# Optimization experiments

Measured on AMD Instinct MI355X. Metric: run time of the kernel, lower is better.

The kernel has to match this reference:

```python
import jax, jax.numpy as jnp
import numpy as np

N_NODES = 50000
N_EDGES = 1500000
D = 512
LN_EPS = 1e-5


def setup_inputs() -> dict:
    key = jax.random.key(0)
    ks = jax.random.split(key, 8)
    scale = 1.0 / np.sqrt(D)
    return {
        "node_feature": jax.random.normal(ks[0], (N_NODES, D), dtype=jnp.float32),
        "edge_index": jax.random.randint(ks[1], (2, N_EDGES), 0, N_NODES, dtype=jnp.int32),
        "W_l": jax.random.uniform(ks[2], (D, D), jnp.float32, -scale, scale),  # neighbor lin
        "b_l": jnp.zeros((D,), jnp.float32),
        "W_r": jax.random.uniform(ks[3], (D, D), jnp.float32, -scale, scale),  # root lin (no bias)
        "gamma": jnp.ones((D,), jnp.float32),
        "beta": jnp.zeros((D,), jnp.float32),
    }


def _layer_norm(x, gamma, beta):
    mu = jnp.mean(x, axis=-1, keepdims=True)
    var = jnp.mean(jnp.square(x - mu), axis=-1, keepdims=True)
    return (x - mu) * jax.lax.rsqrt(var + LN_EPS) * gamma + beta


def reference(node_feature, edge_index, W_l, b_l, W_r, gamma, beta):
    n = node_feature.shape[0]
    residual = node_feature
    h = _layer_norm(node_feature, gamma, beta)
    src, dst = edge_index[0], edge_index[1]
    # mean-aggregate source features at destinations (gather + segment scatter)
    summed = jax.ops.segment_sum(h[src], dst, num_segments=n)  # [N, D]
    cnt = jax.ops.segment_sum(jnp.ones((src.shape[0],), h.dtype), dst, num_segments=n)
    mean = summed / jnp.maximum(cnt, 1.0)[:, None]
    # SAGEConv: lin_l(aggregated) + lin_r(root); bias on lin_l
    out = mean @ W_l.T + b_l + h @ W_r.T
    out = jax.nn.relu(out)
    return out + residual
```

## Files before the change

### kernel.cpp

```cpp
#include <hip/hip_runtime.h>


#define D_DIM 512

typedef __bf16 bf16x8 __attribute__((ext_vector_type(8)));
typedef float f32x4 __attribute__((ext_vector_type(4)));

__device__ __forceinline__ unsigned short f2bf(float f) {
  unsigned u = __float_as_uint(f);
  u += 0x7fffu + ((u >> 16) & 1u);
  return (unsigned short)(u >> 16);
}
__device__ __forceinline__ float bflo(unsigned u) { return __uint_as_float(u << 16); }
__device__ __forceinline__ float bfhi(unsigned u) { return __uint_as_float(u & 0xffff0000u); }
__device__ __forceinline__ unsigned packbf2(float lo, float hi) {
  return (unsigned)f2bf(lo) | ((unsigned)f2bf(hi) << 16);
}

__global__ void ln_kernel(const float* __restrict__ x, const float* __restrict__ gamma,
                          const float* __restrict__ beta, unsigned short* __restrict__ Acat,
                          int n) {
  int lane = threadIdx.x & 63;
  int row = blockIdx.x * 4 + (threadIdx.x >> 6);
  if (row >= n) return;
  const float* xr = x + (size_t)row * D_DIM + lane * 8;
  float4 a = *(const float4*)xr;
  float4 b = *(const float4*)(xr + 4);
  float sum = a.x + a.y + a.z + a.w + b.x + b.y + b.z + b.w;
  float sq = a.x * a.x + a.y * a.y + a.z * a.z + a.w * a.w +
             b.x * b.x + b.y * b.y + b.z * b.z + b.w * b.w;
#pragma unroll
  for (int m = 1; m < 64; m <<= 1) {
    sum += __shfl_xor(sum, m, 64);
    sq  += __shfl_xor(sq, m, 64);
  }
  float mu = sum * (1.0f / D_DIM);
  float var = sq * (1.0f / D_DIM) - mu * mu;
  float rs = rsqrtf(var + 1e-5f);
  const float* gp = gamma + lane * 8;
  const float* bp = beta + lane * 8;
  float4 g0 = *(const float4*)gp, g1 = *(const float4*)(gp + 4);
  float4 e0 = *(const float4*)bp, e1 = *(const float4*)(bp + 4);
  float h0 = (a.x - mu) * rs * g0.x + e0.x;
  float h1 = (a.y - mu) * rs * g0.y + e0.y;
  float h2 = (a.z - mu) * rs * g0.z + e0.z;
  float h3 = (a.w - mu) * rs * g0.w + e0.w;
  float h4 = (b.x - mu) * rs * g1.x + e1.x;
  float h5 = (b.y - mu) * rs * g1.y + e1.y;
  float h6 = (b.z - mu) * rs * g1.z + e1.z;
  float h7 = (b.w - mu) * rs * g1.w + e1.w;
  uint4 st = { packbf2(h0, h1), packbf2(h2, h3), packbf2(h4, h5), packbf2(h6, h7) };
  *(uint4*)(Acat + (size_t)row * 1024 + 512 + lane * 8) = st;
}

__global__ void wconv_kernel(const float* __restrict__ Wl, const float* __restrict__ Wr,
                             unsigned short* __restrict__ Wcat) {
  int id = blockIdx.x * 256 + threadIdx.x;
  int j = id >> 9, k = id & 511;
  Wcat[(size_t)j * 1024 + k] = f2bf(Wl[id]);
  Wcat[(size_t)j * 1024 + 512 + k] = f2bf(Wr[id]);
}

__global__ void zero_kernel(int* __restrict__ p, int n) {
  int i = blockIdx.x * 256 + threadIdx.x;
  if (i < n) p[i] = 0;
}

__global__ void hist_kernel(const int* __restrict__ dst, int nE, int* __restrict__ cnt) {
  int e = blockIdx.x * 256 + threadIdx.x;
  if (e < nE) atomicAdd(&cnt[dst[e]], 1);
}

__global__ void scan1_kernel(const int* __restrict__ cnt, int n,
                             int* __restrict__ excl, int* __restrict__ bsums) {
  __shared__ int wsum[16];
  int gid = blockIdx.x * 1024 + threadIdx.x;
  int lane = threadIdx.x & 63, wave = threadIdx.x >> 6;
  int v = (gid < n) ? cnt[gid] : 0;
  int s = v;
#pragma unroll
  for (int d = 1; d < 64; d <<= 1) {
    int t = __shfl_up(s, d, 64);
    if (lane >= d) s += t;
  }
  if (lane == 63) wsum[wave] = s;
  __syncthreads();
  if (wave == 0) {
    int ws = (lane < 16) ? wsum[lane] : 0;
#pragma unroll
    for (int d = 1; d < 16; d <<= 1) {
      int t = __shfl_up(ws, d, 64);
      if (lane >= d) ws += t;
    }
    if (lane < 16) wsum[lane] = ws;
  }
  __syncthreads();
  int incl = s + ((wave > 0) ? wsum[wave - 1] : 0);
  if (gid < n) excl[gid] = incl - v;
  if (threadIdx.x == 1023) bsums[blockIdx.x] = incl;
}

__global__ void scan2_kernel(int* __restrict__ bsums, int nb) {
  int lane = threadIdx.x;
  int v = (lane < nb) ? bsums[lane] : 0;
  int s = v;
#pragma unroll
  for (int d = 1; d < 64; d <<= 1) {
    int t = __shfl_up(s, d, 64);
    if (lane >= d) s += t;
  }
  if (lane < nb) bsums[lane] = s - v;
}

__global__ void scan3_kernel(int* __restrict__ rowst, int* __restrict__ cur,
                             const int* __restrict__ bsums, int n, int nE) {
  int gid = blockIdx.x * 1024 + threadIdx.x;
  if (gid < n) {
    int r = rowst[gid] + bsums[blockIdx.x];
    rowst[gid] = r;
    cur[gid] = r;
  }
  if (gid == 0) rowst[n] = nE;
}

__global__ void scatter_kernel(const int* __restrict__ src, const int* __restrict__ dst,
                               int nE, int* __restrict__ cur, int* __restrict__ sorted_src) {
  int e = blockIdx.x * 256 + threadIdx.x;
  if (e < nE) {
    int p = atomicAdd(&cur[dst[e]], 1);
    sorted_src[p] = src[e];
  }
}

__device__ __forceinline__ void acc_row(float* acc, uint4 r) {
  acc[0] += bflo(r.x); acc[1] += bfhi(r.x);
  acc[2] += bflo(r.y); acc[3] += bfhi(r.y);
  acc[4] += bflo(r.z); acc[5] += bfhi(r.z);
  acc[6] += bflo(r.w); acc[7] += bfhi(r.w);
}

__global__ void agg_kernel(unsigned short* __restrict__ Acat,
                           const int* __restrict__ rowst,
                           const int* __restrict__ sorted_src, int n) {
  int lane = threadIdx.x & 63;
  int node = blockIdx.x * 4 + (threadIdx.x >> 6);
  if (node >= n) return;
  int s0 = rowst[node], s1 = rowst[node + 1];
  float acc[8] = {0.f, 0.f, 0.f, 0.f, 0.f, 0.f, 0.f, 0.f};
  const unsigned short* hbase = Acat + 512 + lane * 8;
  int e = s0;
  for (; e + 3 < s1; e += 4) {
    int i0 = sorted_src[e], i1 = sorted_src[e + 1];
    int i2 = sorted_src[e + 2], i3 = sorted_src[e + 3];
    uint4 r0 = *(const uint4*)(hbase + (size_t)i0 * 1024);
    uint4 r1 = *(const uint4*)(hbase + (size_t)i1 * 1024);
    uint4 r2 = *(const uint4*)(hbase + (size_t)i2 * 1024);
    uint4 r3 = *(const uint4*)(hbase + (size_t)i3 * 1024);
    acc_row(acc, r0); acc_row(acc, r1); acc_row(acc, r2); acc_row(acc, r3);
  }
  for (; e < s1; ++e) {
    int i0 = sorted_src[e];
    uint4 r0 = *(const uint4*)(hbase + (size_t)i0 * 1024);
    acc_row(acc, r0);
  }
  int deg = s1 - s0;
  float sc = (deg > 0) ? (1.0f / (float)deg) : 0.0f;
  uint4 st = { packbf2(acc[0] * sc, acc[1] * sc), packbf2(acc[2] * sc, acc[3] * sc),
               packbf2(acc[4] * sc, acc[5] * sc), packbf2(acc[6] * sc, acc[7] * sc) };
  *(uint4*)(Acat + (size_t)node * 1024 + lane * 8) = st;
}

__device__ __forceinline__ void async16(const unsigned short* g, char* lds) {
  __builtin_amdgcn_global_load_lds((const __attribute__((address_space(1))) void*)g,
                                   (__attribute__((address_space(3))) void*)lds, 16, 0, 0);
}

__global__ __launch_bounds__(256) void gemm_kernel(
    const unsigned short* __restrict__ A,
    const unsigned short* __restrict__ B,
    const float* __restrict__ bias,
    const float* __restrict__ residual,
    float* __restrict__ out, int M) {
  __shared__ unsigned short sA[128 * 32];
  __shared__ unsigned short sB[128 * 32];
  const int K = 1024;
  int t = threadIdx.x;
  int lane = t & 63, wave = t >> 6;
  int quad = lane >> 4, l16 = lane & 15;
  int mb = blockIdx.x >> 2, nb = blockIdx.x & 3;
  int mBase = mb * 128, nBase = nb * 128;
  int wm = (wave & 1) * 64, wn = (wave >> 1) * 64;

  const unsigned short* gA = A + (size_t)(mBase + (t >> 2)) * K + (t & 3) * 8;
  const unsigned short* gB = B + (size_t)(nBase + (t >> 2)) * K + (t & 3) * 8;
  char* lA0 = (char*)sA + wave * 1024;
  char* lA1 = (char*)sA + 4096 + wave * 1024;
  char* lB0 = (char*)sB + wave * 1024;
  char* lB1 = (char*)sB + 4096 + wave * 1024;

  f32x4 acc[4][4] = {};

  for (int ks = 0; ks < K; ks += 32) {
    __syncthreads();
    async16(gA + ks, lA0);
    async16(gA + (size_t)64 * K + ks, lA1);
    async16(gB + ks, lB0);
    async16(gB + (size_t)64 * K + ks, lB1);
    __syncthreads();
    bf16x8 af[4], bf[4];
#pragma unroll
    for (int i = 0; i < 4; ++i)
      af[i] = *(const bf16x8*)(sA + (wm + i * 16 + l16) * 32 + quad * 8);
#pragma unroll
    for (int j = 0; j < 4; ++j)
      bf[j] = *(const bf16x8*)(sB + (wn + j * 16 + l16) * 32 + quad * 8);
#pragma unroll
    for (int i = 0; i < 4; ++i)
#pragma unroll
      for (int j = 0; j < 4; ++j)
        acc[i][j] = __builtin_amdgcn_mfma_f32_16x16x32_bf16(af[i], bf[j], acc[i][j], 0, 0, 0);
  }

  float biasv[4];
#pragma unroll
  for (int j = 0; j < 4; ++j) biasv[j] = bias[nBase + wn + j * 16 + l16];
#pragma unroll
  for (int i = 0; i < 4; ++i) {
    int gr0 = mBase + wm + i * 16 + quad * 4;
#pragma unroll
    for (int j = 0; j < 4; ++j) {
      int col = nBase + wn + j * 16 + l16;
#pragma unroll
      for (int r = 0; r < 4; ++r) {
        int gr = gr0 + r;
        if (gr < M) {
          size_t idx = (size_t)gr * D_DIM + col;
          float v = acc[i][j][r] + biasv[j];
          out[idx] = fmaxf(v, 0.0f) + residual[idx];
        }
      }
    }
  }
}

extern "C" void kernel_launch(void* const* d_in, const int* in_sizes, int n_in,
                              void* d_out, int out_size, void* d_ws, size_t ws_size,
                              hipStream_t stream) {
  const float* x = (const float*)d_in[0];
  const int* ei = (const int*)d_in[1];
  const float* Wl = (const float*)d_in[2];
  const float* bl = (const float*)d_in[3];
  const float* Wr = (const float*)d_in[4];
  const float* gamma = (const float*)d_in[5];
  const float* beta = (const float*)d_in[6];
  float* out = (float*)d_out;

  int n = in_sizes[0] / D_DIM;
  int nE = in_sizes[1] / 2;
  const int* src = ei;
  const int* dstv = ei + nE;
  int Mpad = (n + 127) & ~127;

  char* w = (char*)d_ws;
  size_t off = 0;
  auto carve = [&](size_t bytes) {
    char* p = w + off;
    off += (bytes + 255) & ~(size_t)255;
    return p;
  };
  unsigned short* Acat = (unsigned short*)carve((size_t)Mpad * 1024 * 2);
  unsigned short* Wcat = (unsigned short*)carve((size_t)512 * 1024 * 2);
  int* sorted = (int*)carve((size_t)nE * 4);
  int* cnt = (int*)carve((size_t)n * 4);
  int* rowst = (int*)carve((size_t)(n + 1) * 4);
  int* cur = (int*)carve((size_t)n * 4);
  int* bsums = (int*)carve(1024);
  if (off > ws_size) return;

  int nbScan = (n + 1023) / 1024;

  ln_kernel<<<(n + 3) / 4, 256, 0, stream>>>(x, gamma, beta, Acat, n);
  wconv_kernel<<<(512 * 512) / 256, 256, 0, stream>>>(Wl, Wr, Wcat);
  zero_kernel<<<(n + 255) / 256, 256, 0, stream>>>(cnt, n);
  hist_kernel<<<(nE + 255) / 256, 256, 0, stream>>>(dstv, nE, cnt);
  scan1_kernel<<<nbScan, 1024, 0, stream>>>(cnt, n, rowst, bsums);
  scan2_kernel<<<1, 64, 0, stream>>>(bsums, nbScan);
  scan3_kernel<<<nbScan, 1024, 0, stream>>>(rowst, cur, bsums, n, nE);
  scatter_kernel<<<(nE + 255) / 256, 256, 0, stream>>>(src, dstv, nE, cur, sorted);
  agg_kernel<<<(n + 3) / 4, 256, 0, stream>>>(Acat, rowst, sorted, n);
  gemm_kernel<<<(Mpad / 128) * 4, 256, 0, stream>>>(Acat, Wcat, bl, x, out, n);
}
```

Measured before the change: 736.4 us.

## Gather neighbor features from an FP8 copy of normalized features during aggregation

```diff
diff --git a/kernel.cpp b/kernel.cpp
--- a/kernel.cpp
+++ b/kernel.cpp
@@ -5,6 +5,7 @@
 
 typedef __bf16 bf16x8 __attribute__((ext_vector_type(8)));
 typedef float f32x4 __attribute__((ext_vector_type(4)));
+typedef float f32x2 __attribute__((ext_vector_type(2)));
 
 __device__ __forceinline__ unsigned short f2bf(float f) {
   unsigned u = __float_as_uint(f);
@@ -19,7 +20,7 @@
 
 __global__ void ln_kernel(const float* __restrict__ x, const float* __restrict__ gamma,
                           const float* __restrict__ beta, unsigned short* __restrict__ Acat,
-                          int n) {
+                          unsigned char* __restrict__ h8, int n, int use_fp8) {
   int lane = threadIdx.x & 63;
   int row = blockIdx.x * 4 + (threadIdx.x >> 6);
   if (row >= n) return;
@@ -51,6 +52,14 @@
   float h7 = (b.w - mu) * rs * g1.w + e1.w;
   uint4 st = { packbf2(h0, h1), packbf2(h2, h3), packbf2(h4, h5), packbf2(h6, h7) };
   *(uint4*)(Acat + (size_t)row * 1024 + 512 + lane * 8) = st;
+  if (use_fp8) {
+    int p0 = __builtin_amdgcn_cvt_pk_fp8_f32(h0, h1, 0, false);
+    p0 = __builtin_amdgcn_cvt_pk_fp8_f32(h2, h3, p0, true);
+    int p1 = __builtin_amdgcn_cvt_pk_fp8_f32(h4, h5, 0, false);
+    p1 = __builtin_amdgcn_cvt_pk_fp8_f32(h6, h7, p1, true);
+    uint2 st2 = { (unsigned)p0, (unsigned)p1 };
+    *(uint2*)(h8 + (size_t)row * 512 + lane * 8) = st2;
+  }
 }
 
 __global__ void wconv_kernel(const float* __restrict__ Wl, const float* __restrict__ Wr,
@@ -132,36 +141,63 @@
   }
 }
 
-__device__ __forceinline__ void acc_row(float* acc, uint4 r) {
+__device__ __forceinline__ void acc_bf(float* acc, uint4 r) {
   acc[0] += bflo(r.x); acc[1] += bfhi(r.x);
   acc[2] += bflo(r.y); acc[3] += bfhi(r.y);
   acc[4] += bflo(r.z); acc[5] += bfhi(r.z);
   acc[6] += bflo(r.w); acc[7] += bfhi(r.w);
 }
 
+__device__ __forceinline__ void acc_f8(float* acc, uint2 r) {
+  f32x2 a = __builtin_amdgcn_cvt_pk_f32_fp8(r.x, false);
+  f32x2 b = __builtin_amdgcn_cvt_pk_f32_fp8(r.x, true);
+  f32x2 c = __builtin_amdgcn_cvt_pk_f32_fp8(r.y, false);
+  f32x2 d = __builtin_amdgcn_cvt_pk_f32_fp8(r.y, true);
+  acc[0] += a.x; acc[1] += a.y; acc[2] += b.x; acc[3] += b.y;
+  acc[4] += c.x; acc[5] += c.y; acc[6] += d.x; acc[7] += d.y;
+}
+
 __global__ void agg_kernel(unsigned short* __restrict__ Acat,
+                           const unsigned char* __restrict__ h8,
                            const int* __restrict__ rowst,
-                           const int* __restrict__ sorted_src, int n) {
+                           const int* __restrict__ sorted_src, int n, int use_fp8) {
   int lane = threadIdx.x & 63;
   int node = blockIdx.x * 4 + (threadIdx.x >> 6);
   if (node >= n) return;
   int s0 = rowst[node], s1 = rowst[node + 1];
   float acc[8] = {0.f, 0.f, 0.f, 0.f, 0.f, 0.f, 0.f, 0.f};
-  const unsigned short* hbase = Acat + 512 + lane * 8;
-  int e = s0;
-  for (; e + 3 < s1; e += 4) {
-    int i0 = sorted_src[e], i1 = sorted_src[e + 1];
-    int i2 = sorted_src[e + 2], i3 = sorted_src[e + 3];
-    uint4 r0 = *(const uint4*)(hbase + (size_t)i0 * 1024);
-    uint4 r1 = *(const uint4*)(hbase + (size_t)i1 * 1024);
-    uint4 r2 = *(const uint4*)(hbase + (size_t)i2 * 1024);
-    uint4 r3 = *(const uint4*)(hbase + (size_t)i3 * 1024);
-    acc_row(acc, r0); acc_row(acc, r1); acc_row(acc, r2); acc_row(acc, r3);
-  }
-  for (; e < s1; ++e) {
-    int i0 = sorted_src[e];
-    uint4 r0 = *(const uint4*)(hbase + (size_t)i0 * 1024);
-    acc_row(acc, r0);
+  if (use_fp8) {
+    const unsigned char* hb = h8 + lane * 8;
+    int e = s0;
+    for (; e + 3 < s1; e += 4) {
+      int i0 = sorted_src[e], i1 = sorted_src[e + 1];
+      int i2 = sorted_src[e + 2], i3 = sorted_src[e + 3];
+      uint2 r0 = *(const uint2*)(hb + (size_t)i0 * 512);
+      uint2 r1 = *(const uint2*)(hb + (size_t)i1 * 512);
+      uint2 r2 = *(const uint2*)(hb + (size_t)i2 * 512);
+      uint2 r3 = *(const uint2*)(hb + (size_t)i3 * 512);
+      acc_f8(acc, r0); acc_f8(acc, r1); acc_f8(acc, r2); acc_f8(acc, r3);
+    }
+    for (; e < s1; ++e) {
+      uint2 r0 = *(const uint2*)(hb + (size_t)sorted_src[e] * 512);
+      acc_f8(acc, r0);
+    }
+  } else {
+    const unsigned short* hbase = Acat + 512 + lane * 8;
+    int e = s0;
+    for (; e + 3 < s1; e += 4) {
+      int i0 = sorted_src[e], i1 = sorted_src[e + 1];
+      int i2 = sorted_src[e + 2], i3 = sorted_src[e + 3];
+      uint4 r0 = *(const uint4*)(hbase + (size_t)i0 * 1024);
+      uint4 r1 = *(const uint4*)(hbase + (size_t)i1 * 1024);
+      uint4 r2 = *(const uint4*)(hbase + (size_t)i2 * 1024);
+      uint4 r3 = *(const uint4*)(hbase + (size_t)i3 * 1024);
+      acc_bf(acc, r0); acc_bf(acc, r1); acc_bf(acc, r2); acc_bf(acc, r3);
+    }
+    for (; e < s1; ++e) {
+      uint4 r0 = *(const uint4*)(hbase + (size_t)sorted_src[e] * 1024);
+      acc_bf(acc, r0);
+    }
   }
   int deg = s1 - s0;
   float sc = (deg > 0) ? (1.0f / (float)deg) : 0.0f;
@@ -236,7 +272,8 @@
         if (gr < M) {
           size_t idx = (size_t)gr * D_DIM + col;
           float v = acc[i][j][r] + biasv[j];
-          out[idx] = fmaxf(v, 0.0f) + residual[idx];
+          float rv = __builtin_nontemporal_load(&residual[idx]);
+          __builtin_nontemporal_store(fmaxf(v, 0.0f) + rv, &out[idx]);
         }
       }
     }
@@ -273,20 +310,23 @@
   int* sorted = (int*)carve((size_t)nE * 4);
   int* cnt = (int*)carve((size_t)n * 4);
   int* rowst = (int*)carve((size_t)(n + 1) * 4);
-  int* cur = (int*)carve((size_t)n * 4);
   int* bsums = (int*)carve(1024);
   if (off > ws_size) return;
 
+  size_t h8_bytes = (size_t)n * 512;
+  int use_fp8 = (off + h8_bytes <= ws_size) ? 1 : 0;
+  unsigned char* h8 = use_fp8 ? (unsigned char*)carve(h8_bytes) : (unsigned char*)w;
+
   int nbScan = (n + 1023) / 1024;
 
-  ln_kernel<<<(n + 3) / 4, 256, 0, stream>>>(x, gamma, beta, Acat, n);
+  ln_kernel<<<(n + 3) / 4, 256, 0, stream>>>(x, gamma, beta, Acat, h8, n, use_fp8);
   wconv_kernel<<<(512 * 512) / 256, 256, 0, stream>>>(Wl, Wr, Wcat);
   zero_kernel<<<(n + 255) / 256, 256, 0, stream>>>(cnt, n);
   hist_kernel<<<(nE + 255) / 256, 256, 0, stream>>>(dstv, nE, cnt);
   scan1_kernel<<<nbScan, 1024, 0, stream>>>(cnt, n, rowst, bsums);
   scan2_kernel<<<1, 64, 0, stream>>>(bsums, nbScan);
-  scan3_kernel<<<nbScan, 1024, 0, stream>>>(rowst, cur, bsums, n, nE);
-  scatter_kernel<<<(nE + 255) / 256, 256, 0, stream>>>(src, dstv, nE, cur, sorted);
-  agg_kernel<<<(n + 3) / 4, 256, 0, stream>>>(Acat, rowst, sorted, n);
+  scan3_kernel<<<nbScan, 1024, 0, stream>>>(rowst, cnt, bsums, n, nE);
+  scatter_kernel<<<(nE + 255) / 256, 256, 0, stream>>>(src, dstv, nE, cnt, sorted);
+  agg_kernel<<<(n + 3) / 4, 256, 0, stream>>>(Acat, h8, rowst, sorted, n, use_fp8);
   gemm_kernel<<<(Mpad / 128) * 4, 256, 0, stream>>>(Acat, Wcat, bl, x, out, n);
 }
```

Result: faster. 652.3 us (-11.4%).
